# Kernel tuning notes

Measured on AMD Instinct MI355X. Metric: run time of the kernel, lower is better.

## Reference

```python
import jax, jax.numpy as jnp
import numpy as np

N_NODES = 20000
N_EDGES = 160000
N_GRAPHS = 64
HIDDEN = 128
CTX = 2048
HEADS = 4
NUM_LAYERS = 3
NUM_BINS = 240
MAX_DIST = 30.0
GAMMA = 0.5
BN_EPS = 1e-5
OUT_DIM = 1024


def setup_inputs() -> dict:
    key = jax.random.key(0)
    ks = jax.random.split(key, 32)
    inp = {}
    inp["atom_types"] = jax.random.randint(ks[0], (N_NODES,), 0, 118)
    inp["pos"] = jax.random.normal(ks[1], (N_NODES, 3), dtype=jnp.float32) * 5.0
    inp["edge_index"] = jax.random.randint(ks[2], (2, N_EDGES), 0, N_NODES)
    inp["edge_attr"] = jax.random.uniform(ks[3], (N_EDGES, 5), dtype=jnp.float32)
    inp["batch"] = jnp.sort(jax.random.randint(ks[4], (N_NODES,), 0, N_GRAPHS))
    inp["context_vector"] = jax.random.normal(ks[5], (N_GRAPHS, CTX), dtype=jnp.float32)
    # initial node embedding Linear(118 -> 128)
    inp["emb_W"] = jax.random.normal(ks[6], (118, HIDDEN), dtype=jnp.float32) * 0.05
    inp["emb_b"] = jnp.zeros((HIDDEN,), jnp.float32)
    # RBF positional MLP: Linear(720->128) + BN + ReLU + Linear(128->2048)
    inp["rbf_lin1_W"] = jax.random.normal(ks[7], (3 * NUM_BINS, 128), dtype=jnp.float32) * 0.03
    inp["rbf_lin1_b"] = jnp.zeros((128,), jnp.float32)
    inp["rbf_bn_g"] = jnp.ones((128,), jnp.float32)
    inp["rbf_bn_b"] = jnp.zeros((128,), jnp.float32)
    inp["rbf_bn_m"] = jax.random.normal(ks[8], (128,), dtype=jnp.float32) * 0.1
    inp["rbf_bn_v"] = jax.random.uniform(ks[9], (128,), dtype=jnp.float32, minval=0.5, maxval=1.5)
    inp["rbf_lin2_W"] = jax.random.normal(ks[10], (128, CTX), dtype=jnp.float32) * 0.05
    inp["rbf_lin2_b"] = jnp.zeros((CTX,), jnp.float32)
    # per-layer GAT params (stacked over layers)
    in_dim = HIDDEN + CTX  # 2176
    inp["gat_W"] = jax.random.normal(ks[11], (NUM_LAYERS, in_dim, HEADS * HIDDEN), dtype=jnp.float32) * 0.02
    inp["att_src"] = jax.random.normal(ks[12], (NUM_LAYERS, HEADS, HIDDEN), dtype=jnp.float32) * 0.1
    inp["att_dst"] = jax.random.normal(ks[13], (NUM_LAYERS, HEADS, HIDDEN), dtype=jnp.float32) * 0.1
    inp["gat_bias"] = jnp.zeros((NUM_LAYERS, HIDDEN), jnp.float32)
    inp["bn_g"] = jnp.ones((NUM_LAYERS, HIDDEN), jnp.float32)
    inp["bn_b"] = jnp.zeros((NUM_LAYERS, HIDDEN), jnp.float32)
    inp["bn_m"] = jax.random.normal(ks[14], (NUM_LAYERS, HIDDEN), dtype=jnp.float32) * 0.1
    inp["bn_v"] = jax.random.uniform(ks[15], (NUM_LAYERS, HIDDEN), dtype=jnp.float32, minval=0.5, maxval=1.5)
    # final Linear(128 -> 1024)
    inp["out_W"] = jax.random.normal(ks[16], (HIDDEN, OUT_DIM), dtype=jnp.float32) * 0.05
    inp["out_b"] = jnp.zeros((OUT_DIM,), jnp.float32)
    return inp


def _bn_eval(x, g, b, m, v):
    return (x - m) * jax.lax.rsqrt(v + BN_EPS) * g + b


def _forward(atom_types, pos, edge_index, edge_attr, batch, context_vector,
             emb_W, emb_b, rbf_lin1_W, rbf_lin1_b, rbf_bn_g, rbf_bn_b, rbf_bn_m,
             rbf_bn_v, rbf_lin2_W, rbf_lin2_b, gat_W, att_src, att_dst, gat_bias,
             bn_g, bn_b, bn_m, bn_v, out_W, out_b):
    N = atom_types.shape[0]
    # initial node embedding (one-hot @ W == row gather, but keep faithful math)
    x = jax.nn.one_hot(atom_types, 118, dtype=jnp.float32) @ emb_W + emb_b  # [N,128]
    # RBF positional encoding: [N,3,num_bins] -> [N,720]
    mu = jnp.linspace(-MAX_DIST, MAX_DIST, NUM_BINS, dtype=jnp.float32)
    rbf = jnp.exp(-GAMMA * (pos[..., None] - mu) ** 2).reshape(N, 3 * NUM_BINS)
    h = jax.nn.relu(_bn_eval(rbf @ rbf_lin1_W + rbf_lin1_b, rbf_bn_g, rbf_bn_b, rbf_bn_m, rbf_bn_v))
    pos_emb = h @ rbf_lin2_W + rbf_lin2_b  # [N,2048]
    context = context_vector[batch] + pos_emb  # pos_info == 'add'
    # GAT adds self-loops by default; edge_attr is ignored (edge_dim=None)
    loops = jnp.arange(N)
    src = jnp.concatenate([edge_index[0], loops])  # message source j
    dst = jnp.concatenate([edge_index[1], loops])  # message target i
    for l in range(NUM_LAYERS):
        xc = jnp.concatenate([x, context], axis=1)                  # [N,2176]
        xs = (xc @ gat_W[l]).reshape(N, HEADS, HIDDEN)              # [N,H,C]
        a_src = jnp.einsum('nhc,hc->nh', xs, att_src[l])            # [N,H]
        a_dst = jnp.einsum('nhc,hc->nh', xs, att_dst[l])
        alpha = jax.nn.leaky_relu(a_src[src] + a_dst[dst], 0.2)     # [E+N,H]
        amax = jax.ops.segment_max(alpha, dst, num_segments=N)
        alpha = jnp.exp(alpha - amax[dst])
        denom = jax.ops.segment_sum(alpha, dst, num_segments=N)
        alpha = alpha / jnp.maximum(denom[dst], 1e-16)
        msg = xs[src] * alpha[..., None]                             # [E+N,H,C]
        agg = jax.ops.segment_sum(msg, dst, num_segments=N)          # [N,H,C]
        x_conv = agg.mean(axis=1) + gat_bias[l]                      # concat=False -> head mean
        x_conv = _bn_eval(x_conv, bn_g[l], bn_b[l], bn_m[l], bn_v[l])
        x_conv = jax.nn.gelu(x_conv, approximate=False)
        x = x + x_conv                                               # residual; dropout inactive (eval)
    out = x @ out_W + out_b                                          # [N,1024]
    return jax.ops.segment_sum(out, batch, num_segments=N_GRAPHS)    # global_add_pool -> [B,1024]


def reference(atom_types, pos, edge_index, edge_attr, batch, context_vector,
              emb_W, emb_b, rbf_lin1_W, rbf_lin1_b, rbf_bn_g, rbf_bn_b, rbf_bn_m,
              rbf_bn_v, rbf_lin2_W, rbf_lin2_b, gat_W, att_src, att_dst, gat_bias,
              bn_g, bn_b, bn_m, bn_v, out_W, out_b):
    return _forward(atom_types, pos, edge_index, edge_attr, batch, context_vector,
                    emb_W, emb_b, rbf_lin1_W, rbf_lin1_b, rbf_bn_g, rbf_bn_b,
                    rbf_bn_m, rbf_bn_v, rbf_lin2_W, rbf_lin2_b, gat_W, att_src,
                    att_dst, gat_bias, bn_g, bn_b, bn_m, bn_v, out_W, out_b)
```

## Files before the change

### kernel.cpp

```cpp
#include <hip/hip_runtime.h>
#include <hip/hip_bf16.h>
#include <cstdint>

constexpr int HIDDEN = 128, CTXD = 2048, HEADS = 4, NLAYERS = 3;
constexpr int KRBF = 720, KPAD = 736;
constexpr int KXH = 256;

typedef __bf16 bf16x8 __attribute__((ext_vector_type(8)));
typedef float f32x4 __attribute__((ext_vector_type(4)));

static __device__ __forceinline__ unsigned short f2bf(float f) {
    union { float f; unsigned u; } v; v.f = f;
    unsigned r = v.u + 0x7fffu + ((v.u >> 16) & 1u);
    return (unsigned short)(r >> 16);
}
static __device__ __forceinline__ float bf2f(unsigned short s) {
    union { unsigned u; float f; } v; v.u = ((unsigned)s) << 16; return v.f;
}

__global__ __launch_bounds__(256) void k_misc(const float* __restrict__ W1,
                                              unsigned short* __restrict__ W1t,
                                              const float* __restrict__ W2,
                                              unsigned short* __restrict__ W2bf,
                                              const float* __restrict__ ctx,
                                              const float* __restrict__ b2,
                                              unsigned short* __restrict__ cpre,
                                              int* __restrict__ cnt,
                                              const int* __restrict__ at,
                                              const float* __restrict__ embW,
                                              const float* __restrict__ embB,
                                              float* __restrict__ x,
                                              unsigned short* __restrict__ xh,
                                              const float* __restrict__ gatW,
                                              unsigned short* __restrict__ gatWt,
                                              int N, int NG,
                                              int e0, int e1, int e2, int e3, int e4) {
    __shared__ unsigned short t[32][34];
    int b = blockIdx.x, tid = threadIdx.x;
    if (b < e0) {
        int i = b * 256 + tid;
        if (i < 128 * KPAD) {
            int c = i / KPAD, k = i % KPAD;
            W1t[i] = (k < KRBF) ? f2bf(W1[(size_t)k * 128 + c]) : (unsigned short)0;
        }
    } else if (b < e1) {
        int i = (b - e0) * 256 + tid;
        if (i < 128 * CTXD) W2bf[i] = f2bf(W2[i]);
    } else if (b < e2) {
        int i = (b - e1) * 256 + tid;
        if (i < NG * CTXD) cpre[i] = f2bf(ctx[i] + b2[i % CTXD]);
    } else if (b < e3) {
        int i = (b - e2) * 256 + tid;
        if (i < N) cnt[i] = 1;
    } else if (b < e4) {
        int i = (b - e3) * 256 + tid;
        if (i < N * HIDDEN) {
            int n = i >> 7, c = i & 127;
            float v = embW[(size_t)at[n] * HIDDEN + c] + embB[c];
            x[i] = v;
            xh[(size_t)n * KXH + c] = f2bf(v);
        }
    } else {
        int idx = b - e4;
        int bz = idx / (16 * 68);
        int rem = idx % (16 * 68);
        int bx = rem % 16, by = rem / 16;
        int tx = tid & 31, ty = tid >> 5;
        const int R = 2176, C = 512;
        int c0 = bx * 32, r0 = by * 32;
        const float* s = gatW + (size_t)bz * R * C;
        unsigned short* d = gatWt + (size_t)bz * R * C;
        for (int rr = ty; rr < 32; rr += 8) {
            int r = r0 + rr, c = c0 + tx;
            t[rr][tx] = f2bf(s[(size_t)r * C + c]);
        }
        __syncthreads();
        for (int rr = ty; rr < 32; rr += 8) {
            int c = c0 + rr, r = r0 + tx;
            d[(size_t)c * R + r] = t[tx][rr];
        }
    }
}

template <int MODE>
__device__ __forceinline__ void gemm_core(unsigned short* As, unsigned short* Bs,
                                          const unsigned short* __restrict__ A, int lda, int M,
                                          const unsigned short* __restrict__ Bt, int ldb, int K,
                                          void* __restrict__ Cout, int ldc,
                                          int m0, int n0) {
    constexpr int LDT = 40;
    const int tid = threadIdx.x;
    const int lane = tid & 63, wid = tid >> 6;
    const int wr = (wid >> 1) * 64, wc = (wid & 1) * 64;
    const int sr = tid >> 1, sk = (tid & 1) * 16;
    f32x4 acc[4][4];
#pragma unroll
    for (int i = 0; i < 4; i++)
#pragma unroll
        for (int j = 0; j < 4; j++)
#pragma unroll
            for (int r = 0; r < 4; r++) acc[i][j][r] = 0.f;
    const int nst = K / 32;
    const int arow = min(m0 + sr, M - 1);
    const unsigned short* ap = A + (size_t)arow * lda + sk;
    const unsigned short* bp = Bt + (size_t)(n0 + sr) * ldb + sk;
    uint4 av0 = *(const uint4*)ap, av1 = *(const uint4*)(ap + 8);
    uint4 bv0 = *(const uint4*)bp, bv1 = *(const uint4*)(bp + 8);
    const int fr = lane & 15, kg = lane >> 4;
    for (int ks = 0; ks < nst; ++ks) {
        __syncthreads();
        *(uint4*)&As[sr * LDT + sk] = av0;
        *(uint4*)&As[sr * LDT + sk + 8] = av1;
        *(uint4*)&Bs[sr * LDT + sk] = bv0;
        *(uint4*)&Bs[sr * LDT + sk + 8] = bv1;
        __syncthreads();
        if (ks + 1 < nst) {
            const unsigned short* ap2 = A + (size_t)arow * lda + (ks + 1) * 32 + sk;
            const unsigned short* bp2 = Bt + (size_t)(n0 + sr) * ldb + (ks + 1) * 32 + sk;
            av0 = *(const uint4*)ap2; av1 = *(const uint4*)(ap2 + 8);
            bv0 = *(const uint4*)bp2; bv1 = *(const uint4*)(bp2 + 8);
        }
        bf16x8 afr[4], bfr[4];
#pragma unroll
        for (int i = 0; i < 4; i++) {
            afr[i] = *reinterpret_cast<const bf16x8*>(&As[(wr + i * 16 + fr) * LDT + kg * 8]);
            bfr[i] = *reinterpret_cast<const bf16x8*>(&Bs[(wc + i * 16 + fr) * LDT + kg * 8]);
        }
#pragma unroll
        for (int i = 0; i < 4; i++)
#pragma unroll
            for (int j = 0; j < 4; j++)
                acc[i][j] = __builtin_amdgcn_mfma_f32_16x16x32_bf16(afr[i], bfr[j], acc[i][j], 0, 0, 0);
    }
    const int rg = lane >> 4;
#pragma unroll
    for (int i = 0; i < 4; i++) {
#pragma unroll
        for (int j = 0; j < 4; j++) {
            int col = n0 + wc + j * 16 + fr;
#pragma unroll
            for (int r = 0; r < 4; r++) {
                int row = m0 + wr + i * 16 + rg * 4 + r;
                if (row < M) {
                    float vv = acc[i][j][r];
                    if (MODE == 2) {
                        ((float*)Cout)[(size_t)row * ldc + col] = vv;
                    } else {
                        ((unsigned short*)Cout)[(size_t)row * ldc + col] = f2bf(vv);
                    }
                }
            }
        }
    }
}

__global__ __launch_bounds__(256) void k_rbfprep(const float* __restrict__ pos,
                                                 const unsigned short* __restrict__ W1t,
                                                 const float* __restrict__ b1,
                                                 const float* __restrict__ g,
                                                 const float* __restrict__ bb,
                                                 const float* __restrict__ bm,
                                                 const float* __restrict__ bv,
                                                 unsigned short* __restrict__ xh,
                                                 const unsigned short* __restrict__ gatWt,
                                                 const unsigned short* __restrict__ W2bf,
                                                 const unsigned short* __restrict__ cpre,
                                                 unsigned short* __restrict__ Bc,
                                                 float* __restrict__ cW,
                                                 int N, int NG, int nbRbf) {
    constexpr int LDT = 40;
    __shared__ unsigned short As[128 * LDT];
    __shared__ unsigned short Bs[128 * LDT];
    __shared__ float ps[128 * 3];
    const int bid = blockIdx.x;
    const int tid = threadIdx.x;
    if (bid >= nbRbf) {
        int idx = bid - nbRbf;
        if (idx < 12) {
            int z = idx >> 2, mt = idx & 3;
            gemm_core<0>(As, Bs, gatWt + (size_t)z * 512 * 2176 + 128, 2176, 512,
                         W2bf, CTXD, CTXD, Bc + (size_t)z * 512 * KXH + 128, KXH,
                         mt * 128, 0);
        } else if (idx < 24) {
            int z = (idx - 12) >> 2, nt = (idx - 12) & 3;
            gemm_core<2>(As, Bs, cpre, CTXD, NG, gatWt + (size_t)z * 512 * 2176 + 128, 2176,
                         CTXD, cW + (size_t)z * NG * 512, 512, 0, nt * 128);
        } else {
            int i = (idx - 24) * 256 + tid;
            if (i < NLAYERS * 512 * 128) {
                int lo = i >> 7, k = i & 127;
                Bc[(size_t)lo * KXH + k] = gatWt[(size_t)lo * 2176 + k];
            }
        }
        return;
    }
    const int lane = tid & 63, wid = tid >> 6;
    const int nb = bid * 128;
    for (int i = tid; i < 384; i += 256) {
        int n = nb + i / 3;
        ps[i] = (n < N) ? pos[(size_t)n * 3 + (i % 3)] : 1.0e9f;
    }
    __syncthreads();
    const int sr = tid >> 1, sk = (tid & 1) * 16;
    const int wr = (wid >> 1) * 64, wc = (wid & 1) * 64;
    const int fr = lane & 15, kg = lane >> 4;
    f32x4 acc[4][4];
#pragma unroll
    for (int i = 0; i < 4; i++)
#pragma unroll
        for (int j = 0; j < 4; j++)
#pragma unroll
            for (int r = 0; r < 4; r++) acc[i][j][r] = 0.f;
    const float p0 = ps[sr * 3], p1 = ps[sr * 3 + 1], p2 = ps[sr * 3 + 2];
    const unsigned short* bp = W1t + (size_t)sr * KPAD + sk;
    uint4 bv0 = *(const uint4*)bp, bv1 = *(const uint4*)(bp + 8);
    constexpr int NST = KPAD / 32;
    for (int ks = 0; ks < NST; ++ks) {
        unsigned short av[16];
#pragma unroll
        for (int j = 0; j < 16; j++) {
            int kglob = ks * 32 + sk + j;
            float v = 0.f;
            if (kglob < KRBF) {
                int d = kglob / 240, bin = kglob % 240;
                float mu = -30.f + (60.f / 239.f) * (float)bin;
                float p = (d == 0) ? p0 : ((d == 1) ? p1 : p2);
                float df = p - mu;
                v = __expf(-0.5f * df * df);
            }
            av[j] = f2bf(v);
        }
        __syncthreads();
        *(uint4*)&As[sr * LDT + sk] = *(const uint4*)&av[0];
        *(uint4*)&As[sr * LDT + sk + 8] = *(const uint4*)&av[8];
        *(uint4*)&Bs[sr * LDT + sk] = bv0;
        *(uint4*)&Bs[sr * LDT + sk + 8] = bv1;
        __syncthreads();
        if (ks + 1 < NST) {
            const unsigned short* bp2 = W1t + (size_t)sr * KPAD + (ks + 1) * 32 + sk;
            bv0 = *(const uint4*)bp2;
            bv1 = *(const uint4*)(bp2 + 8);
        }
        bf16x8 afr[4], bfr[4];
#pragma unroll
        for (int i = 0; i < 4; i++) {
            afr[i] = *reinterpret_cast<const bf16x8*>(&As[(wr + i * 16 + fr) * LDT + kg * 8]);
            bfr[i] = *reinterpret_cast<const bf16x8*>(&Bs[(wc + i * 16 + fr) * LDT + kg * 8]);
        }
#pragma unroll
        for (int i = 0; i < 4; i++)
#pragma unroll
            for (int j = 0; j < 4; j++)
                acc[i][j] = __builtin_amdgcn_mfma_f32_16x16x32_bf16(afr[i], bfr[j], acc[i][j], 0, 0, 0);
    }
    const int rg = lane >> 4;
#pragma unroll
    for (int i = 0; i < 4; i++) {
#pragma unroll
        for (int j = 0; j < 4; j++) {
            int col = wc + j * 16 + fr;
            float sc = g[col] * rsqrtf(bv[col] + 1e-5f);
            float sh = bb[col] - bm[col] * sc;
            float bc = b1[col];
#pragma unroll
            for (int r = 0; r < 4; r++) {
                int row = nb + wr + i * 16 + rg * 4 + r;
                if (row < N) {
                    float y = (acc[i][j][r] + bc) * sc + sh;
                    y = fmaxf(y, 0.f);
                    xh[(size_t)row * KXH + 128 + col] = f2bf(y);
                }
            }
        }
    }
}

__global__ __launch_bounds__(256) void k_gemm3(const unsigned short* __restrict__ A, int M,
                                               const unsigned short* __restrict__ Bt,
                                               unsigned short* __restrict__ C,
                                               const int* __restrict__ batch,
                                               const float* __restrict__ cw,
                                               const float* __restrict__ att_s,
                                               const float* __restrict__ att_d,
                                               float* __restrict__ a_src,
                                               float* __restrict__ a_dst) {
    constexpr int LDT = 40;
    __shared__ unsigned short As[2][128 * LDT];
    __shared__ unsigned short Bs[2][128 * LDT];
    const int tid = threadIdx.x;
    const int lane = tid & 63, wid = tid >> 6;
    const int m0 = blockIdx.y * 128, n0 = blockIdx.x * 128;
    const int wr = (wid >> 1) * 64, wc = (wid & 1) * 64;
    const int sr = tid >> 1, sk = (tid & 1) * 16;
    f32x4 acc[4][4];
#pragma unroll
    for (int i = 0; i < 4; i++)
#pragma unroll
        for (int j = 0; j < 4; j++)
#pragma unroll
            for (int r = 0; r < 4; r++) acc[i][j][r] = 0.f;
    const int arow = min(m0 + sr, M - 1);
    const unsigned short* ap = A + (size_t)arow * KXH + sk;
    const unsigned short* bp = Bt + (size_t)(n0 + sr) * KXH + sk;
    uint4 av0 = *(const uint4*)ap, av1 = *(const uint4*)(ap + 8);
    uint4 bv0 = *(const uint4*)bp, bv1 = *(const uint4*)(bp + 8);
    const int fr = lane & 15, kg = lane >> 4;
    constexpr int NST = KXH / 32;
    for (int ks = 0; ks < NST; ++ks) {
        unsigned short* as = As[ks & 1];
        unsigned short* bs = Bs[ks & 1];
        *(uint4*)&as[sr * LDT + sk] = av0;
        *(uint4*)&as[sr * LDT + sk + 8] = av1;
        *(uint4*)&bs[sr * LDT + sk] = bv0;
        *(uint4*)&bs[sr * LDT + sk + 8] = bv1;
        __syncthreads();
        if (ks + 1 < NST) {
            av0 = *(const uint4*)(ap + (ks + 1) * 32);
            av1 = *(const uint4*)(ap + (ks + 1) * 32 + 8);
            bv0 = *(const uint4*)(bp + (ks + 1) * 32);
            bv1 = *(const uint4*)(bp + (ks + 1) * 32 + 8);
        }
        bf16x8 afr[4], bfr[4];
#pragma unroll
        for (int i = 0; i < 4; i++) {
            afr[i] = *reinterpret_cast<const bf16x8*>(&as[(wr + i * 16 + fr) * LDT + kg * 8]);
            bfr[i] = *reinterpret_cast<const bf16x8*>(&bs[(wc + i * 16 + fr) * LDT + kg * 8]);
        }
#pragma unroll
        for (int i = 0; i < 4; i++)
#pragma unroll
            for (int j = 0; j < 4; j++)
                acc[i][j] = __builtin_amdgcn_mfma_f32_16x16x32_bf16(afr[i], bfr[j], acc[i][j], 0, 0, 0);
    }
    const int rg = lane >> 4;
    float pssum[4][4], pdsum[4][4];
#pragma unroll
    for (int i = 0; i < 4; i++)
#pragma unroll
        for (int r = 0; r < 4; r++) { pssum[i][r] = 0.f; pdsum[i][r] = 0.f; }
#pragma unroll
    for (int i = 0; i < 4; i++) {
#pragma unroll
        for (int j = 0; j < 4; j++) {
            int col = n0 + wc + j * 16 + fr;
            float asw = att_s[col], adw = att_d[col];
#pragma unroll
            for (int r = 0; r < 4; r++) {
                int row = m0 + wr + i * 16 + rg * 4 + r;
                if (row < M) {
                    float vv = acc[i][j][r] + cw[(size_t)batch[row] * 512 + col];
                    C[(size_t)row * 512 + col] = f2bf(vv);
                    pssum[i][r] += vv * asw;
                    pdsum[i][r] += vv * adw;
                }
            }
        }
    }
    __syncthreads();
    float* lat = (float*)&As[0][0];
#pragma unroll
    for (int i = 0; i < 4; i++) {
#pragma unroll
        for (int r = 0; r < 4; r++) {
            float s = pssum[i][r], d = pdsum[i][r];
#pragma unroll
            for (int dd = 1; dd < 16; dd <<= 1) {
                s += __shfl_xor(s, dd);
                d += __shfl_xor(d, dd);
            }
            if (fr == 0) {
                int k = i * 16 + rg * 4 + r;
                lat[(wid * 64 + k) * 2] = s;
                lat[(wid * 64 + k) * 2 + 1] = d;
            }
        }
    }
    __syncthreads();
    if ((wid & 1) == 0) {
        int k = lane;
        int row = m0 + (wid >> 1) * 64 + k;
        if (row < M) {
            float s = lat[(wid * 64 + k) * 2] + lat[((wid + 1) * 64 + k) * 2];
            float d = lat[(wid * 64 + k) * 2 + 1] + lat[((wid + 1) * 64 + k) * 2 + 1];
            int head = n0 >> 7;
            a_src[(size_t)row * 4 + head] = s;
            a_dst[(size_t)row * 4 + head] = d;
        }
    }
}

__global__ void k_cnt(const int* __restrict__ ei, int E, int* cnt) {
    int i = blockIdx.x * 256 + threadIdx.x;
    if (i < E) atomicAdd(&cnt[ei[E + i]], 1);
}
__global__ __launch_bounds__(1024) void k_scan(const int* __restrict__ cnt, int* __restrict__ rowptr,
                                               int* __restrict__ cursor, int n) {
    __shared__ int wsum[16];
    __shared__ int carry;
    int tid = threadIdx.x, lane = tid & 63, wid = tid >> 6;
    if (tid == 0) carry = 0;
    __syncthreads();
    for (int basei = 0; basei < n; basei += 1024) {
        int i = basei + tid;
        int v = (i < n) ? cnt[i] : 0;
        int s = v;
#pragma unroll
        for (int d = 1; d < 64; d <<= 1) {
            int t = __shfl_up(s, (unsigned)d);
            if (lane >= d) s += t;
        }
        if (lane == 63) wsum[wid] = s;
        __syncthreads();
        if (wid == 0 && lane < 16) {
            int ws = wsum[lane]; int t = ws;
#pragma unroll
            for (int d = 1; d < 16; d <<= 1) {
                int u = __shfl_up(t, (unsigned)d);
                if (lane >= d) t += u;
            }
            wsum[lane] = t - ws;
        }
        __syncthreads();
        int excl = carry + wsum[wid] + (s - v);
        if (i < n) { rowptr[i] = excl; cursor[i] = excl; }
        __syncthreads();
        if (tid == 1023) carry += wsum[15] + s;
        __syncthreads();
    }
    if (tid == 0) rowptr[n] = carry;
}
__global__ void k_fill(const int* __restrict__ ei, int E, int N, int* cursor, int* csrc) {
    int i = blockIdx.x * 256 + threadIdx.x;
    if (i >= E + N) return;
    int s, d;
    if (i < E) { s = ei[i]; d = ei[E + i]; }
    else { s = i - E; d = s; }
    int slot = atomicAdd(&cursor[d], 1);
    csrc[slot] = s;
}

__global__ __launch_bounds__(256) void k_agg(const int* __restrict__ rowptr,
                                             const int* __restrict__ csrc,
                                             const float* __restrict__ asrc,
                                             const float* __restrict__ adstv,
                                             const unsigned short* __restrict__ xs,
                                             const float* __restrict__ gbias,
                                             const float* __restrict__ bg,
                                             const float* __restrict__ bb,
                                             const float* __restrict__ bm,
                                             const float* __restrict__ bv,
                                             float* __restrict__ x,
                                             unsigned short* __restrict__ xh, int N) {
    __shared__ float wsh[4][64][4];
    __shared__ int ssh[4][64];
    int tid = threadIdx.x, lane = tid & 63, wid = tid >> 6;
    int n = blockIdx.x * 4 + wid;
    if (n >= N) return;
    int beg = rowptr[n], end = rowptr[n + 1];
    float4 ad = *(const float4*)(adstv + (size_t)n * 4);
    int nch = (end - beg + 63) >> 6;
    float m0 = -1e30f, m1 = -1e30f, m2 = -1e30f, m3 = -1e30f;
    float s0 = 0.f, s1 = 0.f, s2 = 0.f, s3 = 0.f;
    float a0 = -1e30f, a1 = -1e30f, a2 = -1e30f, a3 = -1e30f;
    int sv = 0;
    for (int base = beg; base < end; base += 64) {
        int idx = base + lane;
        float b0 = -1e30f, b1 = -1e30f, b2 = -1e30f, b3 = -1e30f;
        int s = 0;
        if (idx < end) {
            s = csrc[idx];
            float4 t = *(const float4*)(asrc + (size_t)s * 4);
            b0 = t.x + ad.x; b0 = b0 > 0.f ? b0 : 0.2f * b0;
            b1 = t.y + ad.y; b1 = b1 > 0.f ? b1 : 0.2f * b1;
            b2 = t.z + ad.z; b2 = b2 > 0.f ? b2 : 0.2f * b2;
            b3 = t.w + ad.w; b3 = b3 > 0.f ? b3 : 0.2f * b3;
        }
        float c0 = b0, c1 = b1, c2 = b2, c3 = b3;
#pragma unroll
        for (int d = 1; d < 64; d <<= 1) {
            c0 = fmaxf(c0, __shfl_xor(c0, d));
            c1 = fmaxf(c1, __shfl_xor(c1, d));
            c2 = fmaxf(c2, __shfl_xor(c2, d));
            c3 = fmaxf(c3, __shfl_xor(c3, d));
        }
        float nm0 = fmaxf(m0, c0), nm1 = fmaxf(m1, c1), nm2 = fmaxf(m2, c2), nm3 = fmaxf(m3, c3);
        float e0 = (idx < end) ? __expf(b0 - nm0) : 0.f;
        float e1 = (idx < end) ? __expf(b1 - nm1) : 0.f;
        float e2 = (idx < end) ? __expf(b2 - nm2) : 0.f;
        float e3 = (idx < end) ? __expf(b3 - nm3) : 0.f;
#pragma unroll
        for (int d = 1; d < 64; d <<= 1) {
            e0 += __shfl_xor(e0, d); e1 += __shfl_xor(e1, d);
            e2 += __shfl_xor(e2, d); e3 += __shfl_xor(e3, d);
        }
        s0 = s0 * __expf(m0 - nm0) + e0; m0 = nm0;
        s1 = s1 * __expf(m1 - nm1) + e1; m1 = nm1;
        s2 = s2 * __expf(m2 - nm2) + e2; m2 = nm2;
        s3 = s3 * __expf(m3 - nm3) + e3; m3 = nm3;
        a0 = b0; a1 = b1; a2 = b2; a3 = b3; sv = s;
    }
    float i0 = 1.f / fmaxf(s0, 1e-16f), i1 = 1.f / fmaxf(s1, 1e-16f);
    float i2 = 1.f / fmaxf(s2, 1e-16f), i3 = 1.f / fmaxf(s3, 1e-16f);
    const int h = lane >> 4, c0i = (lane & 15) * 8;
    float acc[8];
#pragma unroll
    for (int j = 0; j < 8; j++) acc[j] = 0.f;
    for (int base = beg; base < end; base += 64) {
        int s; float w0, w1, w2, w3;
        if (nch == 1) {
            s = sv;
            w0 = __expf(a0 - m0) * i0; w1 = __expf(a1 - m1) * i1;
            w2 = __expf(a2 - m2) * i2; w3 = __expf(a3 - m3) * i3;
        } else {
            int idx = base + lane;
            float b0 = -1e30f, b1 = -1e30f, b2 = -1e30f, b3 = -1e30f;
            s = 0;
            if (idx < end) {
                s = csrc[idx];
                float4 t = *(const float4*)(asrc + (size_t)s * 4);
                b0 = t.x + ad.x; b0 = b0 > 0.f ? b0 : 0.2f * b0;
                b1 = t.y + ad.y; b1 = b1 > 0.f ? b1 : 0.2f * b1;
                b2 = t.z + ad.z; b2 = b2 > 0.f ? b2 : 0.2f * b2;
                b3 = t.w + ad.w; b3 = b3 > 0.f ? b3 : 0.2f * b3;
            }
            w0 = __expf(b0 - m0) * i0; w1 = __expf(b1 - m1) * i1;
            w2 = __expf(b2 - m2) * i2; w3 = __expf(b3 - m3) * i3;
        }
        ssh[wid][lane] = s;
        wsh[wid][lane][0] = w0; wsh[wid][lane][1] = w1;
        wsh[wid][lane][2] = w2; wsh[wid][lane][3] = w3;
        int cnt = min(64, end - base);
        int i = 0;
        for (; i + 2 <= cnt; i += 2) {
            int sa = ssh[wid][i], sb = ssh[wid][i + 1];
            float wa = wsh[wid][i][h], wb = wsh[wid][i + 1][h];
            uint4 ra = *(const uint4*)(xs + ((size_t)sa << 9) + (h << 7) + c0i);
            uint4 rb = *(const uint4*)(xs + ((size_t)sb << 9) + (h << 7) + c0i);
            const unsigned short* qa = (const unsigned short*)&ra;
            const unsigned short* qb = (const unsigned short*)&rb;
#pragma unroll
            for (int j = 0; j < 8; j++) acc[j] += wa * bf2f(qa[j]);
#pragma unroll
            for (int j = 0; j < 8; j++) acc[j] += wb * bf2f(qb[j]);
        }
        if (i < cnt) {
            int sa = ssh[wid][i];
            float wa = wsh[wid][i][h];
            uint4 ra = *(const uint4*)(xs + ((size_t)sa << 9) + (h << 7) + c0i);
            const unsigned short* qa = (const unsigned short*)&ra;
#pragma unroll
            for (int j = 0; j < 8; j++) acc[j] += wa * bf2f(qa[j]);
        }
    }
#pragma unroll
    for (int j = 0; j < 8; j++) {
        acc[j] += __shfl_xor(acc[j], 16);
        acc[j] += __shfl_xor(acc[j], 32);
    }
    if (lane < 16) {
#pragma unroll
        for (int j = 0; j < 8; j++) {
            int c = c0i + j;
            float t = acc[j] * 0.25f + gbias[c];
            float sc = bg[c] * rsqrtf(bv[c] + 1e-5f);
            float y = (t - bm[c]) * sc + bb[c];
            float ge = 0.5f * y * (1.f + erff(y * 0.70710678118f));
            float xn = x[(size_t)n * 128 + c] + ge;
            x[(size_t)n * 128 + c] = xn;
            xh[(size_t)n * KXH + c] = f2bf(xn);
        }
    }
}

__global__ __launch_bounds__(256) void k_pool(const float* __restrict__ x,
                                              const int* __restrict__ batch,
                                              const float* __restrict__ W,
                                              const float* __restrict__ bo,
                                              float* __restrict__ out, int N) {
    __shared__ float xg[128];
    __shared__ float tmp[256];
    __shared__ int bounds[2];
    int g = blockIdx.x, tid = threadIdx.x;
    if (tid < 2) {
        int key = g + tid, lo = 0, hi = N;
        while (lo < hi) { int mid = (lo + hi) >> 1; if (batch[mid] < key) lo = mid + 1; else hi = mid; }
        bounds[tid] = lo;
    }
    __syncthreads();
    int s = bounds[0], e = bounds[1];
    int c = tid & 127, rgp = tid >> 7;
    float a = 0.f;
    for (int n = s + rgp; n < e; n += 2) a += x[(size_t)n * 128 + c];
    tmp[tid] = a;
    __syncthreads();
    if (tid < 128) xg[tid] = tmp[tid] + tmp[tid + 128];
    __syncthreads();
    float cntf = (float)(e - s);
    for (int j = tid; j < 1024; j += 256) {
        float o = cntf * bo[j];
        for (int cc = 0; cc < 128; cc++) o += xg[cc] * W[(size_t)cc * 1024 + j];
        out[(size_t)g * 1024 + j] = o;
    }
}

extern "C" void kernel_launch(void* const* d_in, const int* in_sizes, int n_in,
                              void* d_out, int out_size, void* d_ws, size_t ws_size,
                              hipStream_t stream) {
    const int N = in_sizes[0];
    const int E = in_sizes[2] / 2;
    const int NG = in_sizes[5] / CTXD;
    const int* at = (const int*)d_in[0];
    const float* pos = (const float*)d_in[1];
    const int* ei = (const int*)d_in[2];
    const int* batch = (const int*)d_in[4];
    const float* ctx = (const float*)d_in[5];
    const float* embW = (const float*)d_in[6];
    const float* embB = (const float*)d_in[7];
    const float* W1 = (const float*)d_in[8];
    const float* b1 = (const float*)d_in[9];
    const float* rg = (const float*)d_in[10];
    const float* rb = (const float*)d_in[11];
    const float* rm = (const float*)d_in[12];
    const float* rv = (const float*)d_in[13];
    const float* W2 = (const float*)d_in[14];
    const float* b2 = (const float*)d_in[15];
    const float* gatW = (const float*)d_in[16];
    const float* atts = (const float*)d_in[17];
    const float* attd = (const float*)d_in[18];
    const float* gbias = (const float*)d_in[19];
    const float* bg = (const float*)d_in[20];
    const float* bbb = (const float*)d_in[21];
    const float* bm = (const float*)d_in[22];
    const float* bv = (const float*)d_in[23];
    const float* outW = (const float*)d_in[24];
    const float* outb = (const float*)d_in[25];
    float* out = (float*)d_out;

    char* basep = (char*)d_ws;
    size_t off = 0;
    auto alloc = [&](size_t bytes) -> char* {
        char* p = basep + off;
        off = (off + bytes + 255) & ~(size_t)255;
        return p;
    };
    unsigned short* xh = (unsigned short*)alloc((size_t)N * KXH * 2);
    float* x = (float*)alloc((size_t)N * 128 * 4);
    unsigned short* xs = (unsigned short*)alloc((size_t)N * 512 * 2);
    float* a_src = (float*)alloc((size_t)N * 4 * 4);
    float* a_dst = (float*)alloc((size_t)N * 4 * 4);
    int* cnt = (int*)alloc((size_t)N * 4);
    int* rowptr = (int*)alloc((size_t)(N + 1) * 4);
    int* cursor = (int*)alloc((size_t)N * 4);
    int* csrc = (int*)alloc((size_t)(E + N) * 4);
    unsigned short* gatWt = (unsigned short*)alloc((size_t)NLAYERS * 512 * 2176 * 2);
    unsigned short* W1t = (unsigned short*)alloc((size_t)128 * KPAD * 2);
    unsigned short* W2bf = (unsigned short*)alloc((size_t)128 * CTXD * 2);
    unsigned short* cpre = (unsigned short*)alloc((size_t)NG * CTXD * 2);
    unsigned short* Bc = (unsigned short*)alloc((size_t)NLAYERS * 512 * KXH * 2);
    float* cW = (float*)alloc((size_t)NLAYERS * NG * 512 * 4);
    (void)ws_size; (void)n_in; (void)out_size;

    {
        int nbW1t = (128 * KPAD + 255) / 256;
        int nbW2 = (128 * CTXD + 255) / 256;
        int nbCp = (NG * CTXD + 255) / 256;
        int nbCi = (N + 255) / 256;
        int nbEm = (N * 128 + 255) / 256;
        int nbTr = 16 * 68 * 3;
        int e0 = nbW1t, e1 = e0 + nbW2, e2 = e1 + nbCp, e3 = e2 + nbCi, e4 = e3 + nbEm;
        int total = e4 + nbTr;
        k_misc<<<total, 256, 0, stream>>>(W1, W1t, W2, W2bf, ctx, b2, cpre, cnt,
                                          at, embW, embB, x, xh, gatW, gatWt,
                                          N, NG, e0, e1, e2, e3, e4);
    }
    k_cnt<<<(E + 255) / 256, 256, 0, stream>>>(ei, E, cnt);
    {
        int nbRbf = (N + 127) / 128;
        int nbBc = (NLAYERS * 512 * 128 + 255) / 256;
        k_rbfprep<<<nbRbf + 24 + nbBc, 256, 0, stream>>>(pos, W1t, b1, rg, rb, rm, rv, xh,
                                                         gatWt, W2bf, cpre, Bc, cW, N, NG, nbRbf);
    }
    k_scan<<<1, 1024, 0, stream>>>(cnt, rowptr, cursor, N);
    k_fill<<<(E + N + 255) / 256, 256, 0, stream>>>(ei, E, N, cursor, csrc);
    {
        dim3 g(4, (N + 127) / 128, 1);
        for (int l = 0; l < NLAYERS; l++) {
            k_gemm3<<<g, 256, 0, stream>>>(xh, N, Bc + (size_t)l * 512 * KXH,
                                           xs, batch, cW + (size_t)l * NG * 512,
                                           atts + l * 512, attd + l * 512, a_src, a_dst);
            k_agg<<<(N + 3) / 4, 256, 0, stream>>>(rowptr, csrc, a_src, a_dst, xs,
                                                   gbias + l * 128, bg + l * 128, bbb + l * 128,
                                                   bm + l * 128, bv + l * 128, x, xh, N);
        }
    }
    k_pool<<<NG, 256, 0, stream>>>(x, batch, outW, outb, out, N);
}
```

Measured before the change: 434.1 us.

## Double-buffer LDS in gemm_core, XCD-aware tile remap, chunked single-pass scan

gemm_core now alternates between two LDS buffers and drops the leading barrier, so each k-step needs one sync instead of two. k_gemm3 switches to a 1D grid and remaps block IDs so tiles that share A rows stay on the same XCD, aiming for better L2 reuse on MI355X. k_scan changes from a looped block scan to per-thread serial chunks followed by one block-wide scan, removing the multi-iteration barrier loop. The double buffers double the LDS used by k_rbfprep, which may lower its occupancy, and the serial per-thread chunks read memory uncoalesced.

```diff
diff --git a/kernel.cpp b/kernel.cpp
--- a/kernel.cpp
+++ b/kernel.cpp
@@ -83,7 +83,8 @@
 }
 
 template <int MODE>
-__device__ __forceinline__ void gemm_core(unsigned short* As, unsigned short* Bs,
+__device__ __forceinline__ void gemm_core(unsigned short (*As)[128 * 40],
+                                          unsigned short (*Bs)[128 * 40],
                                           const unsigned short* __restrict__ A, int lda, int M,
                                           const unsigned short* __restrict__ Bt, int ldb, int K,
                                           void* __restrict__ Cout, int ldc,
@@ -108,23 +109,24 @@
     uint4 bv0 = *(const uint4*)bp, bv1 = *(const uint4*)(bp + 8);
     const int fr = lane & 15, kg = lane >> 4;
     for (int ks = 0; ks < nst; ++ks) {
-        __syncthreads();
-        *(uint4*)&As[sr * LDT + sk] = av0;
-        *(uint4*)&As[sr * LDT + sk + 8] = av1;
-        *(uint4*)&Bs[sr * LDT + sk] = bv0;
-        *(uint4*)&Bs[sr * LDT + sk + 8] = bv1;
+        unsigned short* as = As[ks & 1];
+        unsigned short* bs = Bs[ks & 1];
+        *(uint4*)&as[sr * LDT + sk] = av0;
+        *(uint4*)&as[sr * LDT + sk + 8] = av1;
+        *(uint4*)&bs[sr * LDT + sk] = bv0;
+        *(uint4*)&bs[sr * LDT + sk + 8] = bv1;
         __syncthreads();
         if (ks + 1 < nst) {
-            const unsigned short* ap2 = A + (size_t)arow * lda + (ks + 1) * 32 + sk;
-            const unsigned short* bp2 = Bt + (size_t)(n0 + sr) * ldb + (ks + 1) * 32 + sk;
-            av0 = *(const uint4*)ap2; av1 = *(const uint4*)(ap2 + 8);
-            bv0 = *(const uint4*)bp2; bv1 = *(const uint4*)(bp2 + 8);
+            av0 = *(const uint4*)(ap + (ks + 1) * 32);
+            av1 = *(const uint4*)(ap + (ks + 1) * 32 + 8);
+            bv0 = *(const uint4*)(bp + (ks + 1) * 32);
+            bv1 = *(const uint4*)(bp + (ks + 1) * 32 + 8);
         }
         bf16x8 afr[4], bfr[4];
 #pragma unroll
         for (int i = 0; i < 4; i++) {
-            afr[i] = *reinterpret_cast<const bf16x8*>(&As[(wr + i * 16 + fr) * LDT + kg * 8]);
-            bfr[i] = *reinterpret_cast<const bf16x8*>(&Bs[(wc + i * 16 + fr) * LDT + kg * 8]);
+            afr[i] = *reinterpret_cast<const bf16x8*>(&as[(wr + i * 16 + fr) * LDT + kg * 8]);
+            bfr[i] = *reinterpret_cast<const bf16x8*>(&bs[(wc + i * 16 + fr) * LDT + kg * 8]);
         }
 #pragma unroll
         for (int i = 0; i < 4; i++)
@@ -169,8 +171,8 @@
                                                  float* __restrict__ cW,
                                                  int N, int NG, int nbRbf) {
     constexpr int LDT = 40;
-    __shared__ unsigned short As[128 * LDT];
-    __shared__ unsigned short Bs[128 * LDT];
+    __shared__ unsigned short As[2][128 * LDT];
+    __shared__ unsigned short Bs[2][128 * LDT];
     __shared__ float ps[128 * 3];
     const int bid = blockIdx.x;
     const int tid = threadIdx.x;
@@ -231,10 +233,10 @@
             av[j] = f2bf(v);
         }
         __syncthreads();
-        *(uint4*)&As[sr * LDT + sk] = *(const uint4*)&av[0];
-        *(uint4*)&As[sr * LDT + sk + 8] = *(const uint4*)&av[8];
-        *(uint4*)&Bs[sr * LDT + sk] = bv0;
-        *(uint4*)&Bs[sr * LDT + sk + 8] = bv1;
+        *(uint4*)&As[0][sr * LDT + sk] = *(const uint4*)&av[0];
+        *(uint4*)&As[0][sr * LDT + sk + 8] = *(const uint4*)&av[8];
+        *(uint4*)&Bs[0][sr * LDT + sk] = bv0;
+        *(uint4*)&Bs[0][sr * LDT + sk + 8] = bv1;
         __syncthreads();
         if (ks + 1 < NST) {
             const unsigned short* bp2 = W1t + (size_t)sr * KPAD + (ks + 1) * 32 + sk;
@@ -244,8 +246,8 @@
         bf16x8 afr[4], bfr[4];
 #pragma unroll
         for (int i = 0; i < 4; i++) {
-            afr[i] = *reinterpret_cast<const bf16x8*>(&As[(wr + i * 16 + fr) * LDT + kg * 8]);
-            bfr[i] = *reinterpret_cast<const bf16x8*>(&Bs[(wc + i * 16 + fr) * LDT + kg * 8]);
+            afr[i] = *reinterpret_cast<const bf16x8*>(&As[0][(wr + i * 16 + fr) * LDT + kg * 8]);
+            bfr[i] = *reinterpret_cast<const bf16x8*>(&Bs[0][(wc + i * 16 + fr) * LDT + kg * 8]);
         }
 #pragma unroll
         for (int i = 0; i < 4; i++)
@@ -289,7 +291,12 @@
     __shared__ unsigned short Bs[2][128 * LDT];
     const int tid = threadIdx.x;
     const int lane = tid & 63, wid = tid >> 6;
-    const int m0 = blockIdx.y * 128, n0 = blockIdx.x * 128;
+    const int nwg = gridDim.x;
+    const int q = nwg >> 3, r = nwg & 7;
+    const int orig = blockIdx.x;
+    const int xcd = orig & 7, slot = orig >> 3;
+    const int tile = (xcd < r) ? (xcd * (q + 1) + slot) : (r * (q + 1) + (xcd - r) * q + slot);
+    const int n0 = (tile & 3) * 128, m0 = (tile >> 2) * 128;
     const int wr = (wid >> 1) * 64, wc = (wid & 1) * 64;
     const int sr = tid >> 1, sk = (tid & 1) * 16;
     f32x4 acc[4][4];
@@ -298,7 +305,7 @@
 #pragma unroll
         for (int j = 0; j < 4; j++)
 #pragma unroll
-            for (int r = 0; r < 4; r++) acc[i][j][r] = 0.f;
+            for (int r2 = 0; r2 < 4; r2++) acc[i][j][r2] = 0.f;
     const int arow = min(m0 + sr, M - 1);
     const unsigned short* ap = A + (size_t)arow * KXH + sk;
     const unsigned short* bp = Bt + (size_t)(n0 + sr) * KXH + sk;
@@ -337,7 +344,7 @@
 #pragma unroll
     for (int i = 0; i < 4; i++)
 #pragma unroll
-        for (int r = 0; r < 4; r++) { pssum[i][r] = 0.f; pdsum[i][r] = 0.f; }
+        for (int r2 = 0; r2 < 4; r2++) { pssum[i][r2] = 0.f; pdsum[i][r2] = 0.f; }
 #pragma unroll
     for (int i = 0; i < 4; i++) {
 #pragma unroll
@@ -345,13 +352,13 @@
             int col = n0 + wc + j * 16 + fr;
             float asw = att_s[col], adw = att_d[col];
 #pragma unroll
-            for (int r = 0; r < 4; r++) {
-                int row = m0 + wr + i * 16 + rg * 4 + r;
+            for (int r2 = 0; r2 < 4; r2++) {
+                int row = m0 + wr + i * 16 + rg * 4 + r2;
                 if (row < M) {
-                    float vv = acc[i][j][r] + cw[(size_t)batch[row] * 512 + col];
+                    float vv = acc[i][j][r2] + cw[(size_t)batch[row] * 512 + col];
                     C[(size_t)row * 512 + col] = f2bf(vv);
-                    pssum[i][r] += vv * asw;
-                    pdsum[i][r] += vv * adw;
+                    pssum[i][r2] += vv * asw;
+                    pdsum[i][r2] += vv * adw;
                 }
             }
         }
@@ -361,15 +368,15 @@
 #pragma unroll
     for (int i = 0; i < 4; i++) {
 #pragma unroll
-        for (int r = 0; r < 4; r++) {
-            float s = pssum[i][r], d = pdsum[i][r];
+        for (int r2 = 0; r2 < 4; r2++) {
+            float s = pssum[i][r2], d = pdsum[i][r2];
 #pragma unroll
             for (int dd = 1; dd < 16; dd <<= 1) {
                 s += __shfl_xor(s, dd);
                 d += __shfl_xor(d, dd);
             }
             if (fr == 0) {
-                int k = i * 16 + rg * 4 + r;
+                int k = i * 16 + rg * 4 + r2;
                 lat[(wid * 64 + k) * 2] = s;
                 lat[(wid * 64 + k) * 2 + 1] = d;
             }
@@ -396,38 +403,37 @@
 __global__ __launch_bounds__(1024) void k_scan(const int* __restrict__ cnt, int* __restrict__ rowptr,
                                                int* __restrict__ cursor, int n) {
     __shared__ int wsum[16];
-    __shared__ int carry;
     int tid = threadIdx.x, lane = tid & 63, wid = tid >> 6;
-    if (tid == 0) carry = 0;
+    int ch = (n + 1023) >> 10;
+    int b = tid * ch, e = min(b + ch, n);
+    if (b > n) b = n;
+    int sum = 0;
+    for (int i = b; i < e; i++) sum += cnt[i];
+    int s = sum;
+#pragma unroll
+    for (int d = 1; d < 64; d <<= 1) {
+        int t = __shfl_up(s, (unsigned)d);
+        if (lane >= d) s += t;
+    }
+    if (lane == 63) wsum[wid] = s;
     __syncthreads();
-    for (int basei = 0; basei < n; basei += 1024) {
-        int i = basei + tid;
-        int v = (i < n) ? cnt[i] : 0;
-        int s = v;
-#pragma unroll
-        for (int d = 1; d < 64; d <<= 1) {
-            int t = __shfl_up(s, (unsigned)d);
-            if (lane >= d) s += t;
-        }
-        if (lane == 63) wsum[wid] = s;
-        __syncthreads();
-        if (wid == 0 && lane < 16) {
-            int ws = wsum[lane]; int t = ws;
-#pragma unroll
-            for (int d = 1; d < 16; d <<= 1) {
-                int u = __shfl_up(t, (unsigned)d);
-                if (lane >= d) t += u;
-            }
-            wsum[lane] = t - ws;
-        }
-        __syncthreads();
-        int excl = carry + wsum[wid] + (s - v);
-        if (i < n) { rowptr[i] = excl; cursor[i] = excl; }
-        __syncthreads();
-        if (tid == 1023) carry += wsum[15] + s;
-        __syncthreads();
-    }
-    if (tid == 0) rowptr[n] = carry;
+    if (wid == 0 && lane < 16) {
+        int ws = wsum[lane]; int t = ws;
+#pragma unroll
+        for (int d = 1; d < 16; d <<= 1) {
+            int u = __shfl_up(t, (unsigned)d);
+            if (lane >= d) t += u;
+        }
+        wsum[lane] = t - ws;
+    }
+    __syncthreads();
+    int run = wsum[wid] + (s - sum);
+    for (int i = b; i < e; i++) {
+        rowptr[i] = run;
+        cursor[i] = run;
+        run += cnt[i];
+    }
+    if (e == n) rowptr[n] = run;
 }
 __global__ void k_fill(const int* __restrict__ ei, int E, int N, int* cursor, int* csrc) {
     int i = blockIdx.x * 256 + threadIdx.x;
@@ -683,11 +689,11 @@
     k_scan<<<1, 1024, 0, stream>>>(cnt, rowptr, cursor, N);
     k_fill<<<(E + N + 255) / 256, 256, 0, stream>>>(ei, E, N, cursor, csrc);
     {
-        dim3 g(4, (N + 127) / 128, 1);
+        int nwg = 4 * ((N + 127) / 128);
         for (int l = 0; l < NLAYERS; l++) {
-            k_gemm3<<<g, 256, 0, stream>>>(xh, N, Bc + (size_t)l * 512 * KXH,
-                                           xs, batch, cW + (size_t)l * NG * 512,
-                                           atts + l * 512, attd + l * 512, a_src, a_dst);
+            k_gemm3<<<nwg, 256, 0, stream>>>(xh, N, Bc + (size_t)l * 512 * KXH,
+                                             xs, batch, cW + (size_t)l * NG * 512,
+                                             atts + l * 512, attd + l * 512, a_src, a_dst);
             k_agg<<<(N + 3) / 4, 256, 0, stream>>>(rowptr, csrc, a_src, a_dst, xs,
                                                    gbias + l * 128, bg + l * 128, bbb + l * 128,
                                                    bm + l * 128, bv + l * 128, x, xh, N);
```

Measured after the change: 440.1 us. No clear change (+1.4%).
